# Kernel tuning notes

Measured on AMD Instinct MI355X. Metric: run time of the kernel, lower is better.

Reference implementation:

```python
import jax, jax.numpy as jnp
import numpy as np

D_MODEL = 1024
NHEAD = 16
HEAD_DIM = D_MODEL // NHEAD
FF = 4096
ALPHA = 1.4142135  # deepnorm_alpha
WIN = (127, 128)   # sliding window (left, right)
EPS = 1e-5
ROPE_BASE = 10000.0


def rmsnorm(x, g):
    ms = jnp.mean(x * x, axis=-1, keepdims=True)
    return x * jax.lax.rsqrt(ms + EPS) * g


def rope(x):
    # x: [B, T, H, D]; non-interleaved rotary over full head dim
    T, D = x.shape[1], x.shape[-1]
    half = D // 2
    inv_freq = 1.0 / (ROPE_BASE ** (jnp.arange(half, dtype=jnp.float32) * 2.0 / D))
    ang = jnp.arange(T, dtype=jnp.float32)[:, None] * inv_freq[None, :]  # [T, half]
    cos = jnp.cos(ang)[None, :, None, :]
    sin = jnp.sin(ang)[None, :, None, :]
    x1, x2 = x[..., :half], x[..., half:]
    return jnp.concatenate([x1 * cos - x2 * sin, x2 * cos + x1 * sin], axis=-1)


def setup_inputs() -> dict:
    key = jax.random.key(0)
    ks = jax.random.split(key, 8)
    d, h = D_MODEL, FF
    return {
        "x": jax.random.normal(ks[0], (2, 2048, d), jnp.float32),
        "Wqkv": jax.random.normal(ks[1], (3 * d, d), jnp.float32) * 0.02,
        "Wout": jax.random.normal(ks[2], (d, d), jnp.float32) * 0.02,
        "bout": jnp.zeros((d,), jnp.float32),
        "W1": jax.random.normal(ks[3], (2 * h, d), jnp.float32) * 0.02,
        "W2": jax.random.normal(ks[4], (d, h), jnp.float32) * 0.02,
        "g1": jnp.ones((d,), jnp.float32),
        "g2": jnp.ones((d,), jnp.float32),
    }


def reference(x, Wqkv, Wout, bout, W1, W2, g1, g2):
    B, T, d = x.shape
    # --- self attention with RoPE + sliding window band mask ---
    qkv = (x @ Wqkv.T).reshape(B, T, 3, NHEAD, HEAD_DIM)
    q, k, v = qkv[:, :, 0], qkv[:, :, 1], qkv[:, :, 2]  # [B,T,H,Dh]
    q = rope(q)
    k = rope(k)
    q = jnp.swapaxes(q, 1, 2)  # [B,H,T,Dh]
    k = jnp.swapaxes(k, 1, 2)
    v = jnp.swapaxes(v, 1, 2)
    scale = 1.0 / np.sqrt(HEAD_DIM)
    scores = jnp.einsum('bhqd,bhkd->bhqk', q, k) * scale
    idx = jnp.arange(T)
    rel = idx[None, :] - idx[:, None]  # j - i
    band = (rel >= -WIN[0]) & (rel <= WIN[1])  # [T,T] allowed positions
    scores = jnp.where(band[None, None], scores, -jnp.inf)
    attn = jax.nn.softmax(scores, axis=-1)
    o = jnp.einsum('bhqk,bhkd->bhqd', attn, v)
    o = jnp.swapaxes(o, 1, 2).reshape(B, T, d)
    a = o @ Wout.T + bout
    # --- deepnorm residual 1 + RMSNorm ---
    x1 = a + ALPHA * x
    x2 = rmsnorm(x1, g1)
    # --- SwiGLU MLP: y, gate = fc1(x).chunk(2); y*gate*sigmoid(gate) ---
    yg = x2 @ W1.T
    y, gate = jnp.split(yg, 2, axis=-1)
    y = y * gate * jax.nn.sigmoid(gate)
    y = y @ W2.T
    # --- deepnorm residual 2 + RMSNorm ---
    x3 = y + ALPHA * x2
    return rmsnorm(x3, g2)
```

## Files before the change

kernel.cpp:

```cpp
#include <hip/hip_runtime.h>

#define T_SEQ   2048
#define NHEADS  16
#define DHEAD   64
#define DMODEL  1024
#define ALPHA_C 1.4142135f
#define EPS_C   1e-5f

typedef __attribute__((ext_vector_type(8))) short bf16x8;
typedef __attribute__((ext_vector_type(4))) short bf16x4;
typedef __attribute__((ext_vector_type(4))) float floatx4;

__device__ __forceinline__ float bf2f(unsigned short u) {
  union { unsigned int i; float f; } v;
  v.i = ((unsigned int)u) << 16;
  return v.f;
}
__device__ __forceinline__ unsigned short f2bf(float f) {
  union { float f; unsigned int i; } v;
  v.f = f;
  unsigned int u = v.i;
  u += 0x7FFF + ((u >> 16) & 1);
  return (unsigned short)(u >> 16);
}

__device__ __forceinline__ void gload_lds16(const void* g, void* l) {
  __builtin_amdgcn_global_load_lds(
      (const __attribute__((address_space(1))) void*)g,
      (__attribute__((address_space(3))) void*)l, 16, 0, 0);
}

__global__ void convert_all(const float* __restrict__ Wqkv,
                            const float* __restrict__ Wout,
                            const float* __restrict__ W1,
                            const float* __restrict__ W2,
                            const float* __restrict__ x,
                            unsigned short* __restrict__ ws)
{
  size_t i = ((size_t)blockIdx.x * 256 + threadIdx.x) * 8;
  const float* src;
  size_t off;
  if      (i <  3145728) { src = Wqkv; off = i; }
  else if (i <  4194304) { src = Wout; off = i -  3145728; }
  else if (i < 12582912) { src = W1;   off = i -  4194304; }
  else if (i < 16777216) { src = W2;   off = i - 12582912; }
  else                   { src = x;    off = i - 16777216; }
  floatx4 a = *(const floatx4*)(src + off);
  floatx4 b = *(const floatx4*)(src + off + 4);
  bf16x8 o;
  #pragma unroll
  for (int u = 0; u < 4; u++) {
    o[u]     = (short)f2bf(a[u]);
    o[4 + u] = (short)f2bf(b[u]);
  }
  *(bf16x8*)(ws + i) = o;
}

__global__ void build_rope_lut(float* __restrict__ cosT,
                               float* __restrict__ sinT)
{
  int gid = blockIdx.x * 256 + threadIdx.x;
  int t = gid >> 5, i = gid & 31;
  float fr = powf(10000.f, -(float)i * (1.f / 32.f));
  float sn, cs;
  sincosf((float)t * fr, &sn, &cs);
  cosT[gid] = cs;
  sinT[gid] = sn;
}

template<int BN>
__global__ __launch_bounds__(256) void gemm_lds(
    const unsigned short* __restrict__ A,
    const unsigned short* __restrict__ W,
    unsigned short* __restrict__ C,
    const float* __restrict__ bias,
    int M, int N, int K, int lda)
{
  constexpr int WN = BN / 2;
  constexpr int NJ = WN / 16;
  __shared__ unsigned short As[128 * 32];
  __shared__ unsigned short Bs[BN * 32];

  const int tid  = threadIdx.x;
  const int lane = tid & 63;
  const int wave = tid >> 6;
  const int wm = (wave >> 1) * 64;
  const int wn = (wave & 1) * WN;
  const int mBase = blockIdx.y * 128;
  const int nBase = blockIdx.x * BN;

  const int sRow = lane >> 2;
  const int sCol = (lane & 3) * 8;

  floatx4 acc[4][NJ];
  #pragma unroll
  for (int i = 0; i < 4; i++)
    #pragma unroll
    for (int j = 0; j < NJ; j++) acc[i][j] = (floatx4){0.f, 0.f, 0.f, 0.f};

  const int mrow = lane & 15;
  const int kq   = (lane >> 4) * 8;

  for (int kb = 0; kb < K; kb += 32) {
    __syncthreads();
    #pragma unroll
    for (int j = 0; j < 2; j++) {
      int r = wave * 32 + j * 16 + sRow;
      gload_lds16(A + (size_t)(mBase + r) * lda + kb + sCol,
                  &As[wave * 1024 + j * 512 + lane * 8]);
    }
    if constexpr (BN == 128) {
      #pragma unroll
      for (int j = 0; j < 2; j++) {
        int r = wave * 32 + j * 16 + sRow;
        gload_lds16(W + (size_t)(nBase + r) * K + kb + sCol,
                    &Bs[wave * 1024 + j * 512 + lane * 8]);
      }
    } else {
      int r = wave * 16 + sRow;
      gload_lds16(W + (size_t)(nBase + r) * K + kb + sCol,
                  &Bs[wave * 512 + lane * 8]);
    }
    __syncthreads();

    bf16x8 af[4], bfr[NJ];
    #pragma unroll
    for (int i = 0; i < 4; i++)
      af[i] = *(const bf16x8*)&As[(wm + i * 16 + mrow) * 32 + kq];
    #pragma unroll
    for (int j = 0; j < NJ; j++)
      bfr[j] = *(const bf16x8*)&Bs[(wn + j * 16 + mrow) * 32 + kq];
    #pragma unroll
    for (int i = 0; i < 4; i++)
      #pragma unroll
      for (int j = 0; j < NJ; j++)
        acc[i][j] = __builtin_amdgcn_mfma_f32_16x16x32_bf16(af[i], bfr[j], acc[i][j], 0, 0, 0);
  }

  const int col0 = lane & 15;
  const int row0 = (lane >> 4) * 4;
  #pragma unroll
  for (int j = 0; j < NJ; j++) {
    const int col = nBase + wn + j * 16 + col0;
    const float badd = bias ? bias[col] : 0.f;
    #pragma unroll
    for (int i = 0; i < 4; i++) {
      #pragma unroll
      for (int r = 0; r < 4; r++) {
        const int row = mBase + wm + i * 16 + row0 + r;
        C[(size_t)row * N + col] = f2bf(acc[i][j][r] + badd);
      }
    }
  }
}

__global__ __launch_bounds__(256) void gemm_qkv_rope(
    const unsigned short* __restrict__ A,
    const unsigned short* __restrict__ W,
    const float* __restrict__ cosT,
    const float* __restrict__ sinT,
    unsigned short* __restrict__ Qd,
    unsigned short* __restrict__ Kd,
    unsigned short* __restrict__ Vd)
{
  constexpr int K = 1024;
  __shared__ unsigned short As[128 * 32];
  __shared__ unsigned short Bs[128 * 32];

  const int tid  = threadIdx.x;
  const int lane = tid & 63;
  const int wave = tid >> 6;
  const int wm = (wave >> 1) * 64;
  const int wn = (wave & 1) * 64;
  const int mBase = blockIdx.y * 128;
  const int nBase = blockIdx.x * 128;

  const int sRow = lane >> 2;
  const int sCol = (lane & 3) * 8;

  floatx4 acc[4][4];
  #pragma unroll
  for (int i = 0; i < 4; i++)
    #pragma unroll
    for (int j = 0; j < 4; j++) acc[i][j] = (floatx4){0.f, 0.f, 0.f, 0.f};

  const int mrow = lane & 15;
  const int kq   = (lane >> 4) * 8;

  for (int kb = 0; kb < K; kb += 32) {
    __syncthreads();
    #pragma unroll
    for (int j = 0; j < 2; j++) {
      int r = wave * 32 + j * 16 + sRow;
      gload_lds16(A + (size_t)(mBase + r) * K + kb + sCol,
                  &As[wave * 1024 + j * 512 + lane * 8]);
      gload_lds16(W + (size_t)(nBase + r) * K + kb + sCol,
                  &Bs[wave * 1024 + j * 512 + lane * 8]);
    }
    __syncthreads();

    bf16x8 af[4], bfr[4];
    #pragma unroll
    for (int i = 0; i < 4; i++) {
      af[i]  = *(const bf16x8*)&As[(wm + i * 16 + mrow) * 32 + kq];
      bfr[i] = *(const bf16x8*)&Bs[(wn + i * 16 + mrow) * 32 + kq];
    }
    #pragma unroll
    for (int i = 0; i < 4; i++)
      #pragma unroll
      for (int j = 0; j < 4; j++)
        acc[i][j] = __builtin_amdgcn_mfma_f32_16x16x32_bf16(af[i], bfr[j], acc[i][j], 0, 0, 0);
  }

  const int col0 = lane & 15;
  const int row0 = (lane >> 4) * 4;
  const int colBase = nBase + wn;
  const int sect = colBase >> 10;
  const int h    = (colBase & 1023) >> 6;
  unsigned short* dst = (sect == 0) ? Qd : (sect == 1) ? Kd : Vd;

  if (sect < 2) {
    #pragma unroll
    for (int it = 0; it < 4; it++) {
      #pragma unroll
      for (int r = 0; r < 4; r++) {
        const int row = mBase + wm + it * 16 + row0 + r;
        const int b = row >> 11, t = row & 2047;
        size_t ob = ((size_t)((b * NHEADS + h) * T_SEQ + t)) * DHEAD;
        const int tb = t * 32;
        float c0 = cosT[tb + col0],      s0 = sinT[tb + col0];
        float c1 = cosT[tb + col0 + 16], s1 = sinT[tb + col0 + 16];
        float x1a = acc[it][0][r], x2a = acc[it][2][r];
        float x1b = acc[it][1][r], x2b = acc[it][3][r];
        dst[ob + col0]      = f2bf(x1a * c0 - x2a * s0);
        dst[ob + col0 + 32] = f2bf(x2a * c0 + x1a * s0);
        dst[ob + col0 + 16] = f2bf(x1b * c1 - x2b * s1);
        dst[ob + col0 + 48] = f2bf(x2b * c1 + x1b * s1);
      }
    }
  } else {
    #pragma unroll
    for (int it = 0; it < 4; it++)
      #pragma unroll
      for (int j = 0; j < 4; j++)
        #pragma unroll
        for (int r = 0; r < 4; r++) {
          const int row = mBase + wm + it * 16 + row0 + r;
          const int b = row >> 11, t = row & 2047;
          dst[((size_t)((b * NHEADS + h) * T_SEQ + t)) * DHEAD + j * 16 + col0] =
              f2bf(acc[it][j][r]);
        }
  }
}

#define BAR() __builtin_amdgcn_s_barrier()
#define SCB() __builtin_amdgcn_sched_barrier(0)

#define RD_A_S(bb, mh, s)                                                 \
  _Pragma("unroll") for (int i = 0; i < 4; i++)                           \
    af[i][s] = *(const bf16x8*)&lds[(bb) + aRd +                          \
        ((mh) * 64 + i * 16 + mrow) * 64 + (kq0 ^ ((s) << 5))];

#define RD_B_S(bb, s)                                                     \
  _Pragma("unroll") for (int n = 0; n < 4; n++)                           \
    bfr[n][s] = *(const bf16x8*)&lds[(bb) + bRd +                         \
        (bRow0 + n * 16 + mrow) * 64 + (kq0 ^ ((s) << 5))];

#define MFMA8(mh, nh, s)                                                  \
  _Pragma("unroll") for (int i = 0; i < 4; i++)                           \
  _Pragma("unroll") for (int n = 0; n < 2; n++)                           \
    acc[(mh) * 4 + i][(nh) * 2 + n] =                                     \
        __builtin_amdgcn_mfma_f32_16x16x32_bf16(                          \
            af[i][s], bfr[(nh) * 2 + n][s],                               \
            acc[(mh) * 4 + i][(nh) * 2 + n], 0, 0, 0);

__global__ __launch_bounds__(512, 2) void gemm_w1_swiglu_2ph(
    const unsigned short* __restrict__ A,
    const unsigned short* __restrict__ W1,
    unsigned short* __restrict__ ys)
{
  __shared__ unsigned short lds[65536];

  const int tid  = threadIdx.x;
  const int lane = tid & 63;
  const int wid  = tid >> 6;
  const int wr   = wid >> 2;
  const int wc   = wid & 3;
  const int mrow = lane & 15;
  const int quad = lane >> 4;
  const int kq0  = (quad ^ (mrow & 7)) * 8;

  const int bid  = blockIdx.y * 32 + blockIdx.x;
  const int c8   = bid & 7;
  const int u    = bid >> 3;
  const int mBase = ((c8 >> 2) * 8 + (u >> 3)) * 256;
  const int nBase = ((c8 &  3) * 8 + (u &  7)) * 128;

  const int r0 = tid >> 3;
  const int ce = (((tid & 7) ^ (r0 & 7)) * 8);
  const size_t aoff0 = (size_t)(mBase + r0) * 1024 + ce;
  const size_t aoff1 = aoff0 + (size_t)64 * 1024;
  auto growf = [&](int br) {
    int col = nBase + (br >> 6) * 32 + (br & 31);
    return ((br >> 5) & 1) ? 4096 + col : col;
  };
  const size_t boff00 = (size_t)growf(r0)       * 1024 + ce;
  const size_t boff01 = (size_t)growf(64 + r0)  * 1024 + ce;
  const size_t boff10 = (size_t)growf(128 + r0) * 1024 + ce;
  const size_t boff11 = (size_t)growf(192 + r0) * 1024 + ce;
  const int d0 = tid * 8;

  auto stA = [&](int buf, int h, int kt) {
    const unsigned short* g = A + (size_t)kt * 64 + (h ? (size_t)128 * 1024 : 0);
    int base = buf * 32768 + h * 8192;
    gload_lds16(g + aoff0, &lds[base + d0]);
    gload_lds16(g + aoff1, &lds[base + 4096 + d0]);
  };
  auto stB = [&](int buf, int h, int kt) {
    const unsigned short* g = W1 + (size_t)kt * 64;
    int base = buf * 32768 + 16384 + h * 8192;
    gload_lds16(g + (h ? boff10 : boff00), &lds[base + d0]);
    gload_lds16(g + (h ? boff11 : boff01), &lds[base + 4096 + d0]);
  };

  floatx4 acc[8][4];
  #pragma unroll
  for (int i = 0; i < 8; i++)
    #pragma unroll
    for (int n = 0; n < 4; n++) acc[i][n] = (floatx4){0.f, 0.f, 0.f, 0.f};
  bf16x8 af[4][2], bfr[4][2];

  const int aRd   = wr * 8192;
  const int bRd   = 16384 + (wc >> 1) * 8192;
  const int bRow0 = (wc & 1) * 64;

  stB(0, 0, 0); stB(0, 1, 0);
  stA(0, 0, 0); stA(0, 1, 0);
  stB(1, 0, 1); stB(1, 1, 1);
  asm volatile("s_waitcnt vmcnt(4)" ::: "memory");

  for (int t = 0; t < 16; ++t) {
    const int cur = t & 1;
    const int nxt = cur ^ 1;
    const int bb  = cur * 32768;
    const int ta  = (t + 1 < 16) ? t + 1 : 15;
    const int tb  = (t + 2 < 16) ? t + 2 : 15;

    BAR();
    stA(nxt, 0, ta); stA(nxt, 1, ta);
    RD_A_S(bb, 0, 0); RD_B_S(bb, 0);
    SCB();
    RD_A_S(bb, 0, 1); RD_B_S(bb, 1);
    asm volatile("s_waitcnt lgkmcnt(8)" ::: "memory");
    SCB();
    __builtin_amdgcn_s_setprio(1);
    MFMA8(0, 0, 0); MFMA8(0, 1, 0);
    __builtin_amdgcn_s_setprio(0);
    asm volatile("s_waitcnt lgkmcnt(0)" ::: "memory");
    SCB();
    __builtin_amdgcn_s_setprio(1);
    MFMA8(0, 0, 1); MFMA8(0, 1, 1);
    __builtin_amdgcn_s_setprio(0);

    BAR();
    stB(cur, 0, tb); stB(cur, 1, tb);
    RD_A_S(bb, 1, 0);
    SCB();
    RD_A_S(bb, 1, 1);
    asm volatile("s_waitcnt lgkmcnt(4)" ::: "memory");
    SCB();
    __builtin_amdgcn_s_setprio(1);
    MFMA8(1, 0, 0); MFMA8(1, 1, 0);
    __builtin_amdgcn_s_setprio(0);
    asm volatile("s_waitcnt lgkmcnt(0)" ::: "memory");
    SCB();
    __builtin_amdgcn_s_setprio(1);
    MFMA8(1, 0, 1); MFMA8(1, 1, 1);
    __builtin_amdgcn_s_setprio(0);
    asm volatile("s_waitcnt vmcnt(4)" ::: "memory");
  }

  const int col0 = lane & 15;
  const int row0 = (lane >> 4) * 4;
  #pragma unroll
  for (int n = 0; n < 2; n++) {
    const int col = nBase + wc * 32 + n * 16 + col0;
    #pragma unroll
    for (int i = 0; i < 8; i++) {
      const int rowb = mBase + wr * 128 + i * 16 + row0;
      #pragma unroll
      for (int r = 0; r < 4; r++) {
        float y = acc[i][n][r], g = acc[i][n + 2][r];
        float sig = 1.f / (1.f + __expf(-g));
        ys[(size_t)(rowb + r) * 4096 + col] = f2bf(y * g * sig);
      }
    }
  }
  asm volatile("s_waitcnt vmcnt(0)" ::: "memory");
}

#define W2_RD_A(bb, mh, s)                                                \
  _Pragma("unroll") for (int i = 0; i < 2; i++)                           \
    af[i][s] = *(const bf16x8*)&lds[(bb) +                                \
        (wr * 64 + (mh) * 32 + i * 16 + mrow) * 64 + (kq0 ^ ((s) << 5))];

#define W2_RD_B(bb, s)                                                    \
  _Pragma("unroll") for (int n = 0; n < 4; n++)                           \
    bfr[n][s] = *(const bf16x8*)&lds[(bb) + 16384 +                       \
        (wc * 64 + n * 16 + mrow) * 64 + (kq0 ^ ((s) << 5))];

#define W2_MFMA(mh, s)                                                    \
  _Pragma("unroll") for (int i = 0; i < 2; i++)                           \
  _Pragma("unroll") for (int n = 0; n < 4; n++)                           \
    acc[(mh) * 2 + i][n] =                                                \
        __builtin_amdgcn_mfma_f32_16x16x32_bf16(                          \
            af[i][s], bfr[n][s], acc[(mh) * 2 + i][n], 0, 0, 0);

__global__ __launch_bounds__(512, 2) void gemm_w2_2ph(
    const unsigned short* __restrict__ A,
    const unsigned short* __restrict__ W,
    float* __restrict__ Cp)
{
  __shared__ unsigned short lds[49152];

  const int tid  = threadIdx.x;
  const int lane = tid & 63;
  const int wid  = tid >> 6;
  const int wr   = wid >> 1;
  const int wc   = wid & 1;
  const int mrow = lane & 15;
  const int quad = lane >> 4;
  const int kq0  = (quad ^ (mrow & 7)) * 8;

  const int u  = blockIdx.x;
  const int c8 = u & 7;
  const int v  = u >> 3;
  const int zP = v >> 4;
  const int mBase = (((c8 >> 1) & 3) * 4 + ((v >> 2) & 3)) * 256;
  const int nBase = ((c8 & 1) * 4 + (v & 3)) * 128;
  const int kOff  = zP * 2048;

  const int r0 = tid >> 3;
  const int ce = (((tid & 7) ^ (r0 & 7)) * 8);
  const int d0 = tid * 8;

  auto stA = [&](int buf, int h, int kt) {
    const unsigned short* g =
        A + (size_t)(mBase + h * 128 + r0) * 4096 + kOff + kt * 64 + ce;
    int base = buf * 24576 + h * 8192;
    gload_lds16(g, &lds[base + d0]);
    gload_lds16(g + (size_t)64 * 4096, &lds[base + 4096 + d0]);
  };
  auto stB = [&](int buf, int kt) {
    const unsigned short* g =
        W + (size_t)(nBase + r0) * 4096 + kOff + kt * 64 + ce;
    int base = buf * 24576 + 16384;
    gload_lds16(g, &lds[base + d0]);
    gload_lds16(g + (size_t)64 * 4096, &lds[base + 4096 + d0]);
  };

  floatx4 acc[4][4];
  #pragma unroll
  for (int i = 0; i < 4; i++)
    #pragma unroll
    for (int n = 0; n < 4; n++) acc[i][n] = (floatx4){0.f, 0.f, 0.f, 0.f};
  bf16x8 af[2][2], bfr[4][2];

  stB(0, 0);
  stA(0, 0, 0); stA(0, 1, 0);
  stB(1, 1);
  asm volatile("s_waitcnt vmcnt(2)" ::: "memory");

  for (int t = 0; t < 32; ++t) {
    const int cur = t & 1;
    const int nxt = cur ^ 1;
    const int bb  = cur * 24576;
    const int ta  = (t + 1 < 32) ? t + 1 : 31;
    const int tb  = (t + 2 < 32) ? t + 2 : 31;

    BAR();
    stA(nxt, 0, ta); stA(nxt, 1, ta);
    W2_RD_A(bb, 0, 0); W2_RD_B(bb, 0);
    SCB();
    W2_RD_A(bb, 0, 1); W2_RD_B(bb, 1);
    asm volatile("s_waitcnt lgkmcnt(6)" ::: "memory");
    SCB();
    __builtin_amdgcn_s_setprio(1);
    W2_MFMA(0, 0);
    __builtin_amdgcn_s_setprio(0);
    asm volatile("s_waitcnt lgkmcnt(0)" ::: "memory");
    SCB();
    __builtin_amdgcn_s_setprio(1);
    W2_MFMA(0, 1);
    __builtin_amdgcn_s_setprio(0);

    BAR();
    stB(cur, tb);
    W2_RD_A(bb, 1, 0);
    SCB();
    W2_RD_A(bb, 1, 1);
    asm volatile("s_waitcnt lgkmcnt(2)" ::: "memory");
    SCB();
    __builtin_amdgcn_s_setprio(1);
    W2_MFMA(1, 0);
    __builtin_amdgcn_s_setprio(0);
    asm volatile("s_waitcnt lgkmcnt(0)" ::: "memory");
    SCB();
    __builtin_amdgcn_s_setprio(1);
    W2_MFMA(1, 1);
    __builtin_amdgcn_s_setprio(0);
    asm volatile("s_waitcnt vmcnt(2)" ::: "memory");
  }

  const int col0 = lane & 15;
  const int row0 = (lane >> 4) * 4;
  float* dst = Cp + (size_t)zP * 4096 * 1024;
  #pragma unroll
  for (int n = 0; n < 4; n++) {
    const int col = nBase + wc * 64 + n * 16 + col0;
    #pragma unroll
    for (int i = 0; i < 4; i++) {
      const int rowb = mBase + wr * 64 + i * 16 + row0;
      #pragma unroll
      for (int r = 0; r < 4; r++)
        dst[(size_t)(rowb + r) * 1024 + col] = acc[i][n][r];
    }
  }
  asm volatile("s_waitcnt vmcnt(0)" ::: "memory");
}

__global__ __launch_bounds__(256) void attn_mfma(
    const unsigned short* __restrict__ Qg,
    const unsigned short* __restrict__ Kg,
    const unsigned short* __restrict__ Vg,
    unsigned short* __restrict__ Og)
{
  __shared__ unsigned short KV[23040];
  __shared__ unsigned short Qs[64 * 72];
  __shared__ unsigned short Ps[4 * 16 * 328];

  const int tid  = threadIdx.x;
  const int lane = tid & 63;
  const int wave = tid >> 6;
  const int c    = lane & 15;
  const int quad = lane >> 4;
  const int blk  = blockIdx.x;
  const int bh   = blk >> 5;
  const int qBase = (blk & 31) * 64;
  const size_t hbase = (size_t)bh * T_SEQ * DHEAD;

  for (int e = tid; e < 320 * 8; e += 256) {
    int row = e >> 3, ch = e & 7;
    int kg = qBase - 127 + row;
    int kgc = min(max(kg, 0), T_SEQ - 1);
    *(bf16x8*)&KV[row * 72 + ch * 8] =
        *(const bf16x8*)(Kg + hbase + (size_t)kgc * DHEAD + ch * 8);
  }
  for (int e = tid; e < 64 * 8; e += 256) {
    int row = e >> 3, ch = e & 7;
    *(bf16x8*)&Qs[row * 72 + ch * 8] =
        *(const bf16x8*)(Qg + hbase + (size_t)(qBase + row) * DHEAD + ch * 8);
  }
  __syncthreads();

  bf16x8 aq[2];
  #pragma unroll
  for (int hh = 0; hh < 2; hh++)
    aq[hh] = *(const bf16x8*)&Qs[(wave * 16 + c) * 72 + hh * 32 + quad * 8];

  floatx4 s[20];
  #pragma unroll
  for (int kt = 0; kt < 20; kt++) {
    bf16x8 b0 = *(const bf16x8*)&KV[(kt * 16 + c) * 72 + quad * 8];
    bf16x8 b1 = *(const bf16x8*)&KV[(kt * 16 + c) * 72 + 32 + quad * 8];
    floatx4 t = (floatx4){0.f, 0.f, 0.f, 0.f};
    t = __builtin_amdgcn_mfma_f32_16x16x32_bf16(aq[0], b0, t, 0, 0, 0);
    t = __builtin_amdgcn_mfma_f32_16x16x32_bf16(aq[1], b1, t, 0, 0, 0);
    s[kt] = t;
  }
  __syncthreads();

  for (int ch = wave; ch < 5; ch += 4) {
    int koff = ch * 64 + lane;
    int kg = qBase - 127 + koff;
    int kgc = min(max(kg, 0), T_SEQ - 1);
    const unsigned short* vrow = Vg + hbase + (size_t)kgc * DHEAD;
    #pragma unroll
    for (int dg = 0; dg < 8; dg++) {
      bf16x8 v8 = *(const bf16x8*)(vrow + dg * 8);
      #pragma unroll
      for (int j = 0; j < 8; j++)
        KV[(dg * 8 + j) * 328 + koff] = (unsigned short)v8[j];
    }
  }

  const int kLoMin = max(0, 127 - qBase);
  const int kHiMax = min(319, 2047 + 127 - qBase);
  float mx[4] = {-3e38f, -3e38f, -3e38f, -3e38f};
  #pragma unroll
  for (int kt = 0; kt < 20; kt++) {
    const int koff = kt * 16 + c;
    #pragma unroll
    for (int reg = 0; reg < 4; reg++) {
      const int qrow = wave * 16 + quad * 4 + reg;
      const int d = koff - qrow;
      bool ok = (d >= 0) && (d <= 255) && (koff >= kLoMin) && (koff <= kHiMax);
      float val = ok ? s[kt][reg] * 0.125f : -3e38f;
      s[kt][reg] = val;
      mx[reg] = fmaxf(mx[reg], val);
    }
  }
  #pragma unroll
  for (int reg = 0; reg < 4; reg++)
    #pragma unroll
    for (int m = 1; m <= 8; m <<= 1)
      mx[reg] = fmaxf(mx[reg], __shfl_xor(mx[reg], m));

  float ls[4] = {0.f, 0.f, 0.f, 0.f};
  #pragma unroll
  for (int kt = 0; kt < 20; kt++) {
    const int koff = kt * 16 + c;
    #pragma unroll
    for (int reg = 0; reg < 4; reg++) {
      float p = __expf(s[kt][reg] - mx[reg]);
      ls[reg] += p;
      Ps[wave * 5248 + (quad * 4 + reg) * 328 + koff] = f2bf(p);
    }
  }
  float inv[4];
  #pragma unroll
  for (int reg = 0; reg < 4; reg++) {
    #pragma unroll
    for (int m = 1; m <= 8; m <<= 1) ls[reg] += __shfl_xor(ls[reg], m);
    inv[reg] = 1.f / ls[reg];
  }
  __syncthreads();

  floatx4 oacc[4];
  #pragma unroll
  for (int nt = 0; nt < 4; nt++) oacc[nt] = (floatx4){0.f, 0.f, 0.f, 0.f};
  #pragma unroll
  for (int kt2 = 0; kt2 < 10; kt2++) {
    bf16x8 a = *(const bf16x8*)&Ps[wave * 5248 + c * 328 + kt2 * 32 + quad * 8];
    #pragma unroll
    for (int nt = 0; nt < 4; nt++) {
      bf16x8 bb = *(const bf16x8*)&KV[(nt * 16 + c) * 328 + kt2 * 32 + quad * 8];
      oacc[nt] = __builtin_amdgcn_mfma_f32_16x16x32_bf16(a, bb, oacc[nt], 0, 0, 0);
    }
  }

  const int b = bh >> 4, h = bh & 15;
  #pragma unroll
  for (int nt = 0; nt < 4; nt++) {
    #pragma unroll
    for (int reg = 0; reg < 4; reg++) {
      const int qg = qBase + wave * 16 + quad * 4 + reg;
      Og[((size_t)(b * T_SEQ + qg)) * DMODEL + h * DHEAD + nt * 16 + c] =
          f2bf(oacc[nt][reg] * inv[reg]);
    }
  }
}

__global__ __launch_bounds__(256) void rmsnorm_mid(
    const unsigned short* __restrict__ a,
    const float* __restrict__ x,
    const float* __restrict__ g,
    unsigned short* __restrict__ out)
{
  __shared__ float red[4];
  const int row = blockIdx.x;
  const int tid = threadIdx.x;
  const size_t base = (size_t)row * DMODEL;
  const int c = tid * 4;
  bf16x4  av = *(const bf16x4*)(a + base + c);
  floatx4 xv = *(const floatx4*)(x + base + c);
  floatx4 gv = *(const floatx4*)(g + c);
  float s[4], ss = 0.f;
  #pragma unroll
  for (int j = 0; j < 4; j++) {
    s[j] = bf2f((unsigned short)av[j]) + ALPHA_C * xv[j];
    ss += s[j] * s[j];
  }
  #pragma unroll
  for (int m = 1; m <= 32; m <<= 1) ss += __shfl_xor(ss, m);
  if ((tid & 63) == 0) red[tid >> 6] = ss;
  __syncthreads();
  float ms = (red[0] + red[1] + red[2] + red[3]) * (1.f / DMODEL);
  float scl = rsqrtf(ms + EPS_C);
  bf16x4 ov;
  #pragma unroll
  for (int j = 0; j < 4; j++) ov[j] = (short)f2bf(s[j] * scl * gv[j]);
  *(bf16x4*)(out + base + c) = ov;
}

__global__ __launch_bounds__(256) void rmsnorm_final_sk(
    const float* __restrict__ p0,
    const float* __restrict__ p1,
    const unsigned short* __restrict__ x2,
    const float* __restrict__ g,
    float* __restrict__ out)
{
  __shared__ float red[4];
  const int row = blockIdx.x;
  const int tid = threadIdx.x;
  const size_t base = (size_t)row * DMODEL;
  const int c = tid * 4;
  floatx4 a0 = *(const floatx4*)(p0 + base + c);
  floatx4 a1 = *(const floatx4*)(p1 + base + c);
  bf16x4  xv = *(const bf16x4*)(x2 + base + c);
  floatx4 gv = *(const floatx4*)(g + c);
  float s[4], ss = 0.f;
  #pragma unroll
  for (int j = 0; j < 4; j++) {
    s[j] = (a0[j] + a1[j]) + ALPHA_C * bf2f((unsigned short)xv[j]);
    ss += s[j] * s[j];
  }
  #pragma unroll
  for (int m = 1; m <= 32; m <<= 1) ss += __shfl_xor(ss, m);
  if ((tid & 63) == 0) red[tid >> 6] = ss;
  __syncthreads();
  float ms = (red[0] + red[1] + red[2] + red[3]) * (1.f / DMODEL);
  float scl = rsqrtf(ms + EPS_C);
  floatx4 ov;
  #pragma unroll
  for (int j = 0; j < 4; j++) ov[j] = s[j] * scl * gv[j];
  *(floatx4*)(out + base + c) = ov;
}

extern "C" void kernel_launch(void* const* d_in, const int* in_sizes, int n_in,
                              void* d_out, int out_size, void* d_ws, size_t ws_size,
                              hipStream_t stream) {
  (void)in_sizes; (void)n_in; (void)out_size; (void)ws_size;
  const float* x    = (const float*)d_in[0];
  const float* Wqkv = (const float*)d_in[1];
  const float* Wout = (const float*)d_in[2];
  const float* bout = (const float*)d_in[3];
  const float* W1   = (const float*)d_in[4];
  const float* W2   = (const float*)d_in[5];
  const float* g1   = (const float*)d_in[6];
  const float* g2   = (const float*)d_in[7];
  float* out = (float*)d_out;

  unsigned short* ws    = (unsigned short*)d_ws;
  unsigned short* Wqkvb = ws;
  unsigned short* Woutb = ws + 3145728;
  unsigned short* W1b   = ws + 4194304;
  unsigned short* W2b   = ws + 12582912;
  unsigned short* P1    = ws + 16777216;
  unsigned short* x2    = ws + 20971520;
  unsigned short* q     = ws + 25165824;
  unsigned short* k     = ws + 29360128;
  unsigned short* v     = ws + 33554432;
  unsigned short* o     = ws + 37748736;
  unsigned short* ys    = ws + 25165824;
  float* cosT = (float*)(ws + 37748736);
  float* sinT = cosT + 65536;
  float* p0   = (float*)(ws + 41943040);

  build_rope_lut<<<256, 256, 0, stream>>>(cosT, sinT);
  convert_all<<<10240, 256, 0, stream>>>(Wqkv, Wout, W1, W2, x, ws);
  gemm_qkv_rope<<<dim3(24, 32), 256, 0, stream>>>(P1, Wqkvb, cosT, sinT, q, k, v);
  attn_mfma<<<32 * (T_SEQ / 64), 256, 0, stream>>>(q, k, v, o);
  gemm_lds<64><<<dim3(16, 32), 256, 0, stream>>>(o, Woutb, P1, bout, 4096, 1024, 1024, 1024);
  rmsnorm_mid<<<4096, 256, 0, stream>>>(P1, x, g1, x2);
  gemm_w1_swiglu_2ph<<<dim3(32, 16), 512, 0, stream>>>(x2, W1b, ys);
  gemm_w2_2ph<<<256, 512, 0, stream>>>(ys, W2b, p0);
  rmsnorm_final_sk<<<4096, 256, 0, stream>>>(p0, p0 + 4194304, x2, g2, out);
}
```

Measured before the change: 359.3 us.

## Use 256x256 4-phase pipelined GEMM for QKV and W1 SwiGLU kernels

```diff
diff --git a/kernel.cpp b/kernel.cpp
--- a/kernel.cpp
+++ b/kernel.cpp
@@ -154,127 +154,74 @@
   }
 }
 
-__global__ __launch_bounds__(256) void gemm_qkv_rope(
-    const unsigned short* __restrict__ A,
-    const unsigned short* __restrict__ W,
-    const float* __restrict__ cosT,
-    const float* __restrict__ sinT,
-    unsigned short* __restrict__ Qd,
-    unsigned short* __restrict__ Kd,
-    unsigned short* __restrict__ Vd)
-{
-  constexpr int K = 1024;
-  __shared__ unsigned short As[128 * 32];
-  __shared__ unsigned short Bs[128 * 32];
-
-  const int tid  = threadIdx.x;
-  const int lane = tid & 63;
-  const int wave = tid >> 6;
-  const int wm = (wave >> 1) * 64;
-  const int wn = (wave & 1) * 64;
-  const int mBase = blockIdx.y * 128;
-  const int nBase = blockIdx.x * 128;
-
-  const int sRow = lane >> 2;
-  const int sCol = (lane & 3) * 8;
-
-  floatx4 acc[4][4];
-  #pragma unroll
-  for (int i = 0; i < 4; i++)
-    #pragma unroll
-    for (int j = 0; j < 4; j++) acc[i][j] = (floatx4){0.f, 0.f, 0.f, 0.f};
-
-  const int mrow = lane & 15;
-  const int kq   = (lane >> 4) * 8;
-
-  for (int kb = 0; kb < K; kb += 32) {
-    __syncthreads();
-    #pragma unroll
-    for (int j = 0; j < 2; j++) {
-      int r = wave * 32 + j * 16 + sRow;
-      gload_lds16(A + (size_t)(mBase + r) * K + kb + sCol,
-                  &As[wave * 1024 + j * 512 + lane * 8]);
-      gload_lds16(W + (size_t)(nBase + r) * K + kb + sCol,
-                  &Bs[wave * 1024 + j * 512 + lane * 8]);
-    }
-    __syncthreads();
-
-    bf16x8 af[4], bfr[4];
-    #pragma unroll
-    for (int i = 0; i < 4; i++) {
-      af[i]  = *(const bf16x8*)&As[(wm + i * 16 + mrow) * 32 + kq];
-      bfr[i] = *(const bf16x8*)&Bs[(wn + i * 16 + mrow) * 32 + kq];
-    }
-    #pragma unroll
-    for (int i = 0; i < 4; i++)
-      #pragma unroll
-      for (int j = 0; j < 4; j++)
-        acc[i][j] = __builtin_amdgcn_mfma_f32_16x16x32_bf16(af[i], bfr[j], acc[i][j], 0, 0, 0);
-  }
-
-  const int col0 = lane & 15;
-  const int row0 = (lane >> 4) * 4;
-  const int colBase = nBase + wn;
-  const int sect = colBase >> 10;
-  const int h    = (colBase & 1023) >> 6;
-  unsigned short* dst = (sect == 0) ? Qd : (sect == 1) ? Kd : Vd;
-
-  if (sect < 2) {
-    #pragma unroll
-    for (int it = 0; it < 4; it++) {
-      #pragma unroll
-      for (int r = 0; r < 4; r++) {
-        const int row = mBase + wm + it * 16 + row0 + r;
-        const int b = row >> 11, t = row & 2047;
-        size_t ob = ((size_t)((b * NHEADS + h) * T_SEQ + t)) * DHEAD;
-        const int tb = t * 32;
-        float c0 = cosT[tb + col0],      s0 = sinT[tb + col0];
-        float c1 = cosT[tb + col0 + 16], s1 = sinT[tb + col0 + 16];
-        float x1a = acc[it][0][r], x2a = acc[it][2][r];
-        float x1b = acc[it][1][r], x2b = acc[it][3][r];
-        dst[ob + col0]      = f2bf(x1a * c0 - x2a * s0);
-        dst[ob + col0 + 32] = f2bf(x2a * c0 + x1a * s0);
-        dst[ob + col0 + 16] = f2bf(x1b * c1 - x2b * s1);
-        dst[ob + col0 + 48] = f2bf(x2b * c1 + x1b * s1);
-      }
-    }
-  } else {
-    #pragma unroll
-    for (int it = 0; it < 4; it++)
-      #pragma unroll
-      for (int j = 0; j < 4; j++)
-        #pragma unroll
-        for (int r = 0; r < 4; r++) {
-          const int row = mBase + wm + it * 16 + row0 + r;
-          const int b = row >> 11, t = row & 2047;
-          dst[((size_t)((b * NHEADS + h) * T_SEQ + t)) * DHEAD + j * 16 + col0] =
-              f2bf(acc[it][j][r]);
-        }
-  }
-}
-
 #define BAR() __builtin_amdgcn_s_barrier()
 #define SCB() __builtin_amdgcn_sched_barrier(0)
-
-#define RD_A_S(bb, mh, s)                                                 \
+#define LGKM0() do { asm volatile("s_waitcnt lgkmcnt(0)" ::: "memory"); \
+                     __builtin_amdgcn_sched_barrier(0); } while (0)
+
+#define RD_A(bb, mh)                                                      \
   _Pragma("unroll") for (int i = 0; i < 4; i++)                           \
+  _Pragma("unroll") for (int s = 0; s < 2; s++)                           \
     af[i][s] = *(const bf16x8*)&lds[(bb) + aRd +                          \
-        ((mh) * 64 + i * 16 + mrow) * 64 + (kq0 ^ ((s) << 5))];
-
-#define RD_B_S(bb, s)                                                     \
-  _Pragma("unroll") for (int n = 0; n < 4; n++)                           \
-    bfr[n][s] = *(const bf16x8*)&lds[(bb) + bRd +                         \
-        (bRow0 + n * 16 + mrow) * 64 + (kq0 ^ ((s) << 5))];
-
-#define MFMA8(mh, nh, s)                                                  \
+        ((mh) * 64 + i * 16 + mrow) * 64 + (kq0 ^ (s << 5))];
+
+#define RD_B(bb, nh)                                                      \
+  _Pragma("unroll") for (int n = 0; n < 2; n++)                           \
+  _Pragma("unroll") for (int s = 0; s < 2; s++)                           \
+    bf[(nh) * 2 + n][s] = *(const bf16x8*)&lds[(bb) + bRd +               \
+        (bRow0 + ((nh) * 2 + n) * 16 + mrow) * 64 + (kq0 ^ (s << 5))];
+
+#define MFMA16(mh, nh)                                                    \
   _Pragma("unroll") for (int i = 0; i < 4; i++)                           \
   _Pragma("unroll") for (int n = 0; n < 2; n++)                           \
+  _Pragma("unroll") for (int s = 0; s < 2; s++)                           \
     acc[(mh) * 4 + i][(nh) * 2 + n] =                                     \
         __builtin_amdgcn_mfma_f32_16x16x32_bf16(                          \
-            af[i][s], bfr[(nh) * 2 + n][s],                               \
+            af[i][s], bf[(nh) * 2 + n][s],                                \
             acc[(mh) * 4 + i][(nh) * 2 + n], 0, 0, 0);
 
-__global__ __launch_bounds__(512, 2) void gemm_w1_swiglu_2ph(
+#define KLOOP_4PH()                                                       \
+  for (int t = 0; t < 16; ++t) {                                          \
+    const int cur = t & 1;                                                \
+    const int nxt = cur ^ 1;                                              \
+    const int bb  = cur * 32768;                                          \
+    const int ta  = (t + 1 < 16) ? t + 1 : 15;                            \
+    const int tb  = (t + 2 < 16) ? t + 2 : 15;                            \
+                                       \
+    RD_A(bb, 0); RD_B(bb, 0);                                             \
+    stA(nxt, 1, ta);                                                      \
+    BAR(); LGKM0();                                                       \
+    __builtin_amdgcn_s_setprio(1);                                        \
+    MFMA16(0, 0);                                                         \
+    __builtin_amdgcn_s_setprio(0);                                        \
+    BAR();                                                                \
+                                                     \
+    RD_B(bb, 1);                                                          \
+    stB(nxt, 1, ta);                                                      \
+    BAR(); LGKM0();                                                       \
+    __builtin_amdgcn_s_setprio(1);                                        \
+    MFMA16(0, 1);                                                         \
+    __builtin_amdgcn_s_setprio(0);                                        \
+    BAR();                                                                \
+                                                     \
+    RD_A(bb, 1);                                                          \
+    stB(cur, 0, tb);                                                      \
+    BAR(); LGKM0();                                                       \
+    __builtin_amdgcn_s_setprio(1);                                        \
+    MFMA16(1, 1);                                                         \
+    __builtin_amdgcn_s_setprio(0);                                        \
+    BAR();                                                                \
+       \
+    stA(cur, 0, tb);                                                      \
+    BAR(); LGKM0();                                                       \
+    __builtin_amdgcn_s_setprio(1);                                        \
+    MFMA16(1, 0);                                                         \
+    __builtin_amdgcn_s_setprio(0);                                        \
+    asm volatile("s_waitcnt vmcnt(4)" ::: "memory");                      \
+    BAR();                                                                \
+  }
+
+__global__ __launch_bounds__(512, 2) void gemm_w1_swiglu_4ph(
     const unsigned short* __restrict__ A,
     const unsigned short* __restrict__ W1,
     unsigned short* __restrict__ ys)
@@ -290,7 +237,7 @@
   const int quad = lane >> 4;
   const int kq0  = (quad ^ (mrow & 7)) * 8;
 
-  const int bid  = blockIdx.y * 32 + blockIdx.x;
+  const int bid  = blockIdx.x;
   const int c8   = bid & 7;
   const int u    = bid >> 3;
   const int mBase = ((c8 >> 2) * 8 + (u >> 3)) * 256;
@@ -328,57 +275,18 @@
   for (int i = 0; i < 8; i++)
     #pragma unroll
     for (int n = 0; n < 4; n++) acc[i][n] = (floatx4){0.f, 0.f, 0.f, 0.f};
-  bf16x8 af[4][2], bfr[4][2];
+  bf16x8 af[4][2], bf[4][2];
 
   const int aRd   = wr * 8192;
   const int bRd   = 16384 + (wc >> 1) * 8192;
   const int bRow0 = (wc & 1) * 64;
 
-  stB(0, 0, 0); stB(0, 1, 0);
-  stA(0, 0, 0); stA(0, 1, 0);
-  stB(1, 0, 1); stB(1, 1, 1);
+  stB(0, 0, 0); stA(0, 0, 0); stA(0, 1, 0); stB(0, 1, 0);
+  stB(1, 0, 1); stA(1, 0, 1);
   asm volatile("s_waitcnt vmcnt(4)" ::: "memory");
-
-  for (int t = 0; t < 16; ++t) {
-    const int cur = t & 1;
-    const int nxt = cur ^ 1;
-    const int bb  = cur * 32768;
-    const int ta  = (t + 1 < 16) ? t + 1 : 15;
-    const int tb  = (t + 2 < 16) ? t + 2 : 15;
-
-    BAR();
-    stA(nxt, 0, ta); stA(nxt, 1, ta);
-    RD_A_S(bb, 0, 0); RD_B_S(bb, 0);
-    SCB();
-    RD_A_S(bb, 0, 1); RD_B_S(bb, 1);
-    asm volatile("s_waitcnt lgkmcnt(8)" ::: "memory");
-    SCB();
-    __builtin_amdgcn_s_setprio(1);
-    MFMA8(0, 0, 0); MFMA8(0, 1, 0);
-    __builtin_amdgcn_s_setprio(0);
-    asm volatile("s_waitcnt lgkmcnt(0)" ::: "memory");
-    SCB();
-    __builtin_amdgcn_s_setprio(1);
-    MFMA8(0, 0, 1); MFMA8(0, 1, 1);
-    __builtin_amdgcn_s_setprio(0);
-
-    BAR();
-    stB(cur, 0, tb); stB(cur, 1, tb);
-    RD_A_S(bb, 1, 0);
-    SCB();
-    RD_A_S(bb, 1, 1);
-    asm volatile("s_waitcnt lgkmcnt(4)" ::: "memory");
-    SCB();
-    __builtin_amdgcn_s_setprio(1);
-    MFMA8(1, 0, 0); MFMA8(1, 1, 0);
-    __builtin_amdgcn_s_setprio(0);
-    asm volatile("s_waitcnt lgkmcnt(0)" ::: "memory");
-    SCB();
-    __builtin_amdgcn_s_setprio(1);
-    MFMA8(1, 0, 1); MFMA8(1, 1, 1);
-    __builtin_amdgcn_s_setprio(0);
-    asm volatile("s_waitcnt vmcnt(4)" ::: "memory");
-  }
+  BAR();
+
+  KLOOP_4PH();
 
   const int col0 = lane & 15;
   const int row0 = (lane >> 4) * 4;
@@ -395,6 +303,115 @@
         ys[(size_t)(rowb + r) * 4096 + col] = f2bf(y * g * sig);
       }
     }
+  }
+  asm volatile("s_waitcnt vmcnt(0)" ::: "memory");
+}
+
+__global__ __launch_bounds__(512, 2) void gemm_qkv_rope256(
+    const unsigned short* __restrict__ A,
+    const unsigned short* __restrict__ W,
+    const float* __restrict__ cosT,
+    const float* __restrict__ sinT,
+    unsigned short* __restrict__ Qd,
+    unsigned short* __restrict__ Kd,
+    unsigned short* __restrict__ Vd)
+{
+  __shared__ unsigned short lds[65536];
+
+  const int tid  = threadIdx.x;
+  const int lane = tid & 63;
+  const int wid  = tid >> 6;
+  const int wr   = wid >> 2;
+  const int wc   = wid & 3;
+  const int mrow = lane & 15;
+  const int quad = lane >> 4;
+  const int kq0  = (quad ^ (mrow & 7)) * 8;
+
+  const int bid  = blockIdx.x;
+  const int c8   = bid & 7;
+  const int u    = bid >> 3;
+  const int mBase = ((c8 >> 1) * 4 + u / 6) * 256;
+  const int nBase = ((c8 & 1) * 6 + u % 6) * 256;
+
+  const int r0 = tid >> 3;
+  const int ce = (((tid & 7) ^ (r0 & 7)) * 8);
+  const size_t aoff0 = (size_t)(mBase + r0) * 1024 + ce;
+  const size_t aoff1 = aoff0 + (size_t)64 * 1024;
+  const size_t boff00 = (size_t)(nBase + r0)       * 1024 + ce;
+  const size_t boff01 = (size_t)(nBase + 64 + r0)  * 1024 + ce;
+  const size_t boff10 = (size_t)(nBase + 128 + r0) * 1024 + ce;
+  const size_t boff11 = (size_t)(nBase + 192 + r0) * 1024 + ce;
+  const int d0 = tid * 8;
+
+  auto stA = [&](int buf, int h, int kt) {
+    const unsigned short* g = A + (size_t)kt * 64 + (h ? (size_t)128 * 1024 : 0);
+    int base = buf * 32768 + h * 8192;
+    gload_lds16(g + aoff0, &lds[base + d0]);
+    gload_lds16(g + aoff1, &lds[base + 4096 + d0]);
+  };
+  auto stB = [&](int buf, int h, int kt) {
+    const unsigned short* g = W + (size_t)kt * 64;
+    int base = buf * 32768 + 16384 + h * 8192;
+    gload_lds16(g + (h ? boff10 : boff00), &lds[base + d0]);
+    gload_lds16(g + (h ? boff11 : boff01), &lds[base + 4096 + d0]);
+  };
+
+  floatx4 acc[8][4];
+  #pragma unroll
+  for (int i = 0; i < 8; i++)
+    #pragma unroll
+    for (int n = 0; n < 4; n++) acc[i][n] = (floatx4){0.f, 0.f, 0.f, 0.f};
+  bf16x8 af[4][2], bf[4][2];
+
+  const int aRd   = wr * 8192;
+  const int bRd   = 16384 + (wc >> 1) * 8192;
+  const int bRow0 = (wc & 1) * 64;
+
+  stB(0, 0, 0); stA(0, 0, 0); stA(0, 1, 0); stB(0, 1, 0);
+  stB(1, 0, 1); stA(1, 0, 1);
+  asm volatile("s_waitcnt vmcnt(4)" ::: "memory");
+  BAR();
+
+  KLOOP_4PH();
+
+  const int col0 = lane & 15;
+  const int row0 = (lane >> 4) * 4;
+  const int colBase = nBase + wc * 64;
+  const int sect = colBase >> 10;
+  const int h    = (colBase & 1023) >> 6;
+  unsigned short* dst = (sect == 0) ? Qd : (sect == 1) ? Kd : Vd;
+
+  if (sect < 2) {
+    #pragma unroll
+    for (int i = 0; i < 8; i++) {
+      #pragma unroll
+      for (int r = 0; r < 4; r++) {
+        const int row = mBase + wr * 128 + i * 16 + row0 + r;
+        const int b = row >> 11, t = row & 2047;
+        size_t ob = ((size_t)((b * NHEADS + h) * T_SEQ + t)) * DHEAD;
+        const int tb = t * 32;
+        float c0 = cosT[tb + col0],      s0 = sinT[tb + col0];
+        float c1 = cosT[tb + col0 + 16], s1 = sinT[tb + col0 + 16];
+        float x1a = acc[i][0][r], x2a = acc[i][2][r];
+        float x1b = acc[i][1][r], x2b = acc[i][3][r];
+        dst[ob + col0]      = f2bf(x1a * c0 - x2a * s0);
+        dst[ob + col0 + 32] = f2bf(x2a * c0 + x1a * s0);
+        dst[ob + col0 + 16] = f2bf(x1b * c1 - x2b * s1);
+        dst[ob + col0 + 48] = f2bf(x2b * c1 + x1b * s1);
+      }
+    }
+  } else {
+    #pragma unroll
+    for (int i = 0; i < 8; i++)
+      #pragma unroll
+      for (int n = 0; n < 4; n++)
+        #pragma unroll
+        for (int r = 0; r < 4; r++) {
+          const int row = mBase + wr * 128 + i * 16 + row0 + r;
+          const int b = row >> 11, t = row & 2047;
+          dst[((size_t)((b * NHEADS + h) * T_SEQ + t)) * DHEAD + n * 16 + col0] =
+              f2bf(acc[i][n][r]);
+        }
   }
   asm volatile("s_waitcnt vmcnt(0)" ::: "memory");
 }
@@ -759,11 +776,11 @@
 
   build_rope_lut<<<256, 256, 0, stream>>>(cosT, sinT);
   convert_all<<<10240, 256, 0, stream>>>(Wqkv, Wout, W1, W2, x, ws);
-  gemm_qkv_rope<<<dim3(24, 32), 256, 0, stream>>>(P1, Wqkvb, cosT, sinT, q, k, v);
+  gemm_qkv_rope256<<<192, 512, 0, stream>>>(P1, Wqkvb, cosT, sinT, q, k, v);
   attn_mfma<<<32 * (T_SEQ / 64), 256, 0, stream>>>(q, k, v, o);
   gemm_lds<64><<<dim3(16, 32), 256, 0, stream>>>(o, Woutb, P1, bout, 4096, 1024, 1024, 1024);
   rmsnorm_mid<<<4096, 256, 0, stream>>>(P1, x, g1, x2);
-  gemm_w1_swiglu_2ph<<<dim3(32, 16), 512, 0, stream>>>(x2, W1b, ys);
+  gemm_w1_swiglu_4ph<<<512, 512, 0, stream>>>(x2, W1b, ys);
   gemm_w2_2ph<<<256, 512, 0, stream>>>(ys, W2b, p0);
   rmsnorm_final_sk<<<4096, 256, 0, stream>>>(p0, p0 + 4194304, x2, g2, out);
 }
```

Measured after the change: 346.6 us. 1.04x faster.
